# Kernel tuning notes

Hardware: AMD Instinct MI355X
Metric: run time of the kernel (lower is better)

Reference implementation:

```python
import jax, jax.numpy as jnp
import numpy as np
import math


def setup_inputs() -> dict:
    key = jax.random.key(0)
    kq, kk, kv = jax.random.split(key, 3)
    B, H, S, D = 8, 12, 4096, 64
    q = jax.random.normal(kq, (B, H, S, D), dtype=jnp.float32)
    k = jax.random.normal(kk, (B, H, S, D), dtype=jnp.float32)
    v = jax.random.normal(kv, (B, H, S, D), dtype=jnp.float32)
    return {"q": q, "k": k, "v": v}


def reference(q, k, v):
    B, H, S, D = q.shape
    topk = int(2 * math.sqrt(S))  # 128 for S=4096
    # importance = mean + std (torch.std is unbiased -> ddof=1)
    importance = q.mean(axis=-1) + jnp.std(q, axis=-1, ddof=1)  # [B,H,S]
    _, idx = jax.lax.top_k(importance, topk)  # [B,H,topk]
    idx_e = idx[..., None]  # [B,H,topk,1]
    q_s = jnp.take_along_axis(q, idx_e, axis=2)  # [B,H,topk,D]
    k_s = jnp.take_along_axis(k, idx_e, axis=2)
    v_s = jnp.take_along_axis(v, idx_e, axis=2)
    scores = jnp.einsum('bhtd,bhsd->bhts', q_s, k_s) / math.sqrt(D)
    attn = jax.nn.softmax(scores, axis=-1)
    out_s = jnp.einsum('bhts,bhsd->bhtd', attn, v_s)  # [B,H,topk,D]
    # scatter back into a full tensor (torch uses empty_like; we use zeros
    # for the unselected positions so the output is deterministic)
    bI = jnp.arange(B)[:, None, None]
    hI = jnp.arange(H)[None, :, None]
    out = jnp.zeros_like(v).at[bI, hI, idx].set(out_s)  # [B,H,S,D]
    Himg = int(math.sqrt(S))
    return out.reshape(B, -1, Himg, Himg)  # [B, H*D, Himg, Himg]
```

## Files before the change

### kernel.cpp

```cpp
#include <hip/hip_runtime.h>
#include <hip/hip_fp16.h>
#include <math.h>

#define BH_N 96
#define S_N 4096
#define D_N 64
#define TOPK 128

typedef unsigned long long ull;

__device__ __forceinline__ ull orderKey(double d) {
  ull u = (ull)__double_as_longlong(d);
  if (u & 0x8000000000000000ULL) u = ~u;
  else u |= 0x8000000000000000ULL;
  return u;
}

__global__ __launch_bounds__(256)
void imp_zero_kernel(const float* __restrict__ q, float* __restrict__ out,
                     ull* __restrict__ keys) {
  const int tid = threadIdx.x;
  const size_t off = (size_t)blockIdx.x * 1024 + (size_t)tid * 4;
  const float4 v = *reinterpret_cast<const float4*>(q + off);
  float4 z; z.x = z.y = z.z = z.w = 0.f;
  *reinterpret_cast<float4*>(out + off) = z;

  double s  = (double)v.x + (double)v.y + (double)v.z + (double)v.w;
  double ss = (double)v.x * v.x + (double)v.y * v.y +
              (double)v.z * v.z + (double)v.w * v.w;
#pragma unroll
  for (int m = 1; m < 16; m <<= 1) {
    s  += __shfl_xor(s, m, 64);
    ss += __shfl_xor(ss, m, 64);
  }
  if ((tid & 15) == 0) {
    double mean = s * (1.0 / 64.0);
    double var = (ss - s * s * (1.0 / 64.0)) * (1.0 / 63.0);
    if (var < 0.0) var = 0.0;
    keys[(size_t)blockIdx.x * 16 + (tid >> 4)] = orderKey(mean + sqrt(var));
  }
}

__global__ __launch_bounds__(256)
void sel_kernel(const ull* __restrict__ keys, int* __restrict__ idx_out) {
  __shared__ int hist[2][256];
  __shared__ int s_idx[TOPK];
  __shared__ int sD, sRem;
  __shared__ int s_cnt;

  const int tid = threadIdx.x;
  const int lane = tid & 63;
  const int wv = tid >> 6;
  const int bh = blockIdx.x;
  const ull* kb = keys + (size_t)bh * S_N;

  ull key[16];
#pragma unroll
  for (int i = 0; i < 16; ++i) key[i] = kb[i * 256 + tid];

  hist[0][tid] = 0;
  hist[1][tid] = 0;
  if (tid == 0) { s_cnt = 0; }
  __syncthreads();

  ull prefix = 0;
  int rem = TOPK;
  int p = 0;
#pragma unroll 1
  for (int b = 0; b < 8; ++b) {
    const int shift = 56 - 8 * b;
    if (b == 0) {
#pragma unroll
      for (int i = 0; i < 16; ++i)
        atomicAdd(&hist[p][(int)((key[i] >> 56) & 255ULL)], 1);
    } else {
#pragma unroll
      for (int i = 0; i < 16; ++i) {
        if (((key[i] ^ prefix) >> (shift + 8)) == 0)
          atomicAdd(&hist[p][(int)((key[i] >> shift) & 255ULL)], 1);
      }
    }
    __syncthreads();
    if (wv == 0) {
      int rloc = rem;
      for (int c = 0; c < 4; ++c) {
        int d = 255 - (c * 64 + lane);
        int cnt = hist[p][d];
        int pre = cnt;
#pragma unroll
        for (int m = 1; m < 64; m <<= 1) {
          int t = __shfl_up(pre, m, 64);
          if (lane >= m) pre += t;
        }
        int tot = __shfl(pre, 63, 64);
        if (rloc <= tot) {
          ull mask = __ballot(pre >= rloc);
          int l = __ffsll((long long)mask) - 1;
          int preL = __shfl(pre, l, 64);
          int cntL = __shfl(cnt, l, 64);
          if (lane == 0) { sD = 255 - (c * 64 + l); sRem = rloc - (preL - cntL); }
          break;
        }
        rloc -= tot;
      }
    } else {
      for (int j = tid - 64; j < 256; j += 192) hist[p ^ 1][j] = 0;
    }
    __syncthreads();
    prefix |= ((ull)sD) << shift;
    rem = sRem;
    p ^= 1;
  }
  const ull T = prefix;

#pragma unroll
  for (int i = 0; i < 16; ++i) {
    if (key[i] > T) {
      int slot = atomicAdd(&s_cnt, 1);
      s_idx[slot] = i * 256 + tid;
    }
  }
  __syncthreads();
  const int nsel = s_cnt;
  if (wv == 0) {
    int running = 0;
    for (int base = 0; base < S_N && running < rem; base += 64) {
      ull kk2 = kb[base + lane];
      ull mask = __ballot(kk2 == T);
      if (kk2 == T) {
        int below = __popcll(mask & ((1ULL << lane) - 1ULL));
        int pos = running + below;
        if (pos < rem) s_idx[nsel + pos] = base + lane;
      }
      running += __popcll(mask);
    }
  }
  __syncthreads();
  if (tid < TOPK) idx_out[bh * TOPK + tid] = s_idx[tid];
}

__global__ __launch_bounds__(256)
void attn_kernel(const float* __restrict__ q, const float* __restrict__ k,
                 const float* __restrict__ v, const int* __restrict__ idx_all,
                 float* __restrict__ out) {
  __shared__ __align__(16) float sQ[32 * 65];
  __shared__ __align__(16) float sB[64 * 65];
  __shared__ __align__(16) __half sP[32 * 132];
  __shared__ int s_idx[TOPK];

  const int tid = threadIdx.x;
  const int bh = blockIdx.x >> 2;
  const int sub = blockIdx.x & 3;
  if (tid < TOPK) s_idx[tid] = idx_all[bh * TOPK + tid];

  const size_t base = (size_t)bh * S_N * D_N;
  const int rgrp = tid >> 4;
  const int c4 = (tid & 15) * 4;
  const int rr = tid >> 4;
  const int cc = tid & 15;

  __syncthreads();

#pragma unroll
  for (int it = 0; it < 2; ++it) {
    int r = it * 16 + rgrp;
    int srow = s_idx[sub * 32 + r];
    float4 val = *reinterpret_cast<const float4*>(q + base + (size_t)srow * D_N + c4);
    sQ[r * 65 + c4 + 0] = val.x; sQ[r * 65 + c4 + 1] = val.y;
    sQ[r * 65 + c4 + 2] = val.z; sQ[r * 65 + c4 + 3] = val.w;
  }

  float acc[2][8];
#pragma unroll
  for (int j = 0; j < 2; ++j)
#pragma unroll
    for (int m = 0; m < 8; ++m) acc[j][m] = 0.f;

  for (int h = 0; h < 2; ++h) {
    __syncthreads();
#pragma unroll
    for (int it = 0; it < 4; ++it) {
      int r = it * 16 + rgrp;
      int srow = s_idx[h * 64 + r];
      float4 val = *reinterpret_cast<const float4*>(k + base + (size_t)srow * D_N + c4);
      sB[r * 65 + c4 + 0] = val.x; sB[r * 65 + c4 + 1] = val.y;
      sB[r * 65 + c4 + 2] = val.z; sB[r * 65 + c4 + 3] = val.w;
    }
    __syncthreads();
    for (int kk = 0; kk < 64; kk += 2) {
#pragma unroll
      for (int u = 0; u < 2; ++u) {
        float qv0 = sQ[(2 * rr + 0) * 65 + kk + u];
        float qv1 = sQ[(2 * rr + 1) * 65 + kk + u];
        float kv[4];
#pragma unroll
        for (int m = 0; m < 4; ++m) kv[m] = sB[(cc * 4 + m) * 65 + kk + u];
#pragma unroll
        for (int m = 0; m < 4; ++m) {
          acc[0][h * 4 + m] += qv0 * kv[m];
          acc[1][h * 4 + m] += qv1 * kv[m];
        }
      }
    }
  }

  float rmax[2], rsum[2];
#pragma unroll
  for (int j = 0; j < 2; ++j) {
    float mx = acc[j][0];
#pragma unroll
    for (int m = 1; m < 8; ++m) mx = fmaxf(mx, acc[j][m]);
    rmax[j] = mx;
  }
#pragma unroll
  for (int mm = 1; mm < 16; mm <<= 1)
#pragma unroll
    for (int j = 0; j < 2; ++j) rmax[j] = fmaxf(rmax[j], __shfl_xor(rmax[j], mm, 64));
#pragma unroll
  for (int j = 0; j < 2; ++j) {
    float sum = 0.f;
#pragma unroll
    for (int m = 0; m < 8; ++m) {
      float pe = __expf(0.125f * (acc[j][m] - rmax[j]));
      acc[j][m] = pe;
      sum += pe;
    }
    rsum[j] = sum;
  }
#pragma unroll
  for (int mm = 1; mm < 16; mm <<= 1)
#pragma unroll
    for (int j = 0; j < 2; ++j) rsum[j] += __shfl_xor(rsum[j], mm, 64);
#pragma unroll
  for (int j = 0; j < 2; ++j) {
    float rinv = 1.f / rsum[j];
#pragma unroll
    for (int h2 = 0; h2 < 2; ++h2)
#pragma unroll
      for (int m = 0; m < 4; ++m) {
        int col = h2 * 64 + cc * 4 + m;
        sP[(2 * rr + j) * 132 + col] = __float2half_rn(acc[j][h2 * 4 + m] * rinv);
      }
  }

  float acc2[2][4];
#pragma unroll
  for (int j = 0; j < 2; ++j)
#pragma unroll
    for (int m = 0; m < 4; ++m) acc2[j][m] = 0.f;

  for (int h = 0; h < 2; ++h) {
    __syncthreads();
#pragma unroll
    for (int it = 0; it < 4; ++it) {
      int r = it * 16 + rgrp;
      int srow = s_idx[h * 64 + r];
      float4 val = *reinterpret_cast<const float4*>(v + base + (size_t)srow * D_N + c4);
      sB[r * 65 + c4 + 0] = val.x; sB[r * 65 + c4 + 1] = val.y;
      sB[r * 65 + c4 + 2] = val.z; sB[r * 65 + c4 + 3] = val.w;
    }
    __syncthreads();
    for (int s2 = 0; s2 < 64; ++s2) {
      int scol = h * 64 + s2;
      float pj0 = __half2float(sP[(2 * rr + 0) * 132 + scol]);
      float pj1 = __half2float(sP[(2 * rr + 1) * 132 + scol]);
      float vm[4];
#pragma unroll
      for (int m = 0; m < 4; ++m) vm[m] = sB[s2 * 65 + cc * 4 + m];
#pragma unroll
      for (int m = 0; m < 4; ++m) {
        acc2[0][m] += pj0 * vm[m];
        acc2[1][m] += pj1 * vm[m];
      }
    }
  }

#pragma unroll
  for (int j = 0; j < 2; ++j) {
    int srow = s_idx[sub * 32 + 2 * rr + j];
    float4 val;
    val.x = acc2[j][0]; val.y = acc2[j][1]; val.z = acc2[j][2]; val.w = acc2[j][3];
    *reinterpret_cast<float4*>(out + base + (size_t)srow * D_N + cc * 4) = val;
  }
}

extern "C" void kernel_launch(void* const* d_in, const int* in_sizes, int n_in,
                              void* d_out, int out_size, void* d_ws, size_t ws_size,
                              hipStream_t stream) {
  const float* q = (const float*)d_in[0];
  const float* k = (const float*)d_in[1];
  const float* v = (const float*)d_in[2];
  float* out = (float*)d_out;
  ull* keys = (ull*)d_ws;
  int* idx = (int*)((char*)d_ws + (size_t)BH_N * S_N * 8);

  imp_zero_kernel<<<24576, 256, 0, stream>>>(q, out, keys);
  sel_kernel<<<BH_N, 256, 0, stream>>>(keys, idx);
  attn_kernel<<<BH_N * 4, 256, 0, stream>>>(q, k, v, idx, out);
}
```

Baseline: 311.3 us.

## Fuse top-k selection into attention kernel with deterministic ballot compaction

Merges the selection and attention kernels into one launch. Each of the four attention blocks per head recomputes the radix top-k selection redundantly instead of reading indices from a separate kernel. The atomic-based compaction and the serial tie scan over global memory are replaced by ballot-based prefix counting, which gives deterministic ordering. Shared-memory layouts are also changed to a stride-68 padding with transposed K so QK and PV can use float4 LDS reads. The cost is extra shared memory and a 4x duplication of selection work.

```diff
diff --git a/kernel.cpp b/kernel.cpp
--- a/kernel.cpp
+++ b/kernel.cpp
@@ -42,16 +42,22 @@
 }
 
 __global__ __launch_bounds__(256)
-void sel_kernel(const ull* __restrict__ keys, int* __restrict__ idx_out) {
+void fused_attn_kernel(const float* __restrict__ q, const float* __restrict__ k,
+                       const float* __restrict__ v, const ull* __restrict__ keys,
+                       float* __restrict__ out) {
   __shared__ int hist[2][256];
   __shared__ int s_idx[TOPK];
+  __shared__ int cntG[4][16], cntE[4][16];
   __shared__ int sD, sRem;
-  __shared__ int s_cnt;
+  __shared__ __align__(16) float sQ[32 * 68];
+  __shared__ __align__(16) float sKT[64 * 68];
+  __shared__ __align__(16) __half sP[32 * 132];
 
   const int tid = threadIdx.x;
   const int lane = tid & 63;
   const int wv = tid >> 6;
-  const int bh = blockIdx.x;
+  const int bh = blockIdx.x >> 2;
+  const int sub = blockIdx.x & 3;
   const ull* kb = keys + (size_t)bh * S_N;
 
   ull key[16];
@@ -60,7 +66,6 @@
 
   hist[0][tid] = 0;
   hist[1][tid] = 0;
-  if (tid == 0) { s_cnt = 0; }
   __syncthreads();
 
   ull prefix = 0;
@@ -112,46 +117,41 @@
     p ^= 1;
   }
   const ull T = prefix;
+  const int nselG = TOPK - rem;
 
 #pragma unroll
   for (int i = 0; i < 16; ++i) {
-    if (key[i] > T) {
-      int slot = atomicAdd(&s_cnt, 1);
-      s_idx[slot] = i * 256 + tid;
+    ull bg = __ballot(key[i] > T);
+    ull be = __ballot(key[i] == T);
+    if (lane == 0) {
+      cntG[wv][i] = __popcll(bg);
+      cntE[wv][i] = __popcll(be);
     }
   }
   __syncthreads();
-  const int nsel = s_cnt;
-  if (wv == 0) {
-    int running = 0;
-    for (int base = 0; base < S_N && running < rem; base += 64) {
-      ull kk2 = kb[base + lane];
-      ull mask = __ballot(kk2 == T);
-      if (kk2 == T) {
-        int below = __popcll(mask & ((1ULL << lane) - 1ULL));
-        int pos = running + below;
-        if (pos < rem) s_idx[nsel + pos] = base + lane;
-      }
-      running += __popcll(mask);
+  {
+    const ull below = (1ULL << lane) - 1ULL;
+    int baseG = 0, baseE = 0;
+#pragma unroll
+    for (int i = 0; i < 16; ++i) {
+      ull bg = __ballot(key[i] > T);
+      ull be = __ballot(key[i] == T);
+      int offG = baseG, offE = baseE;
+#pragma unroll
+      for (int w = 0; w < 4; ++w) {
+        int cg = cntG[w][i], ce = cntE[w][i];
+        if (w < wv) { offG += cg; offE += ce; }
+        baseG += cg; baseE += ce;
+      }
+      if (key[i] > T) {
+        s_idx[offG + __popcll(bg & below)] = i * 256 + tid;
+      } else if (key[i] == T) {
+        int tr = offE + __popcll(be & below);
+        if (tr < rem) s_idx[nselG + tr] = i * 256 + tid;
+      }
     }
   }
   __syncthreads();
-  if (tid < TOPK) idx_out[bh * TOPK + tid] = s_idx[tid];
-}
-
-__global__ __launch_bounds__(256)
-void attn_kernel(const float* __restrict__ q, const float* __restrict__ k,
-                 const float* __restrict__ v, const int* __restrict__ idx_all,
-                 float* __restrict__ out) {
-  __shared__ __align__(16) float sQ[32 * 65];
-  __shared__ __align__(16) float sB[64 * 65];
-  __shared__ __align__(16) __half sP[32 * 132];
-  __shared__ int s_idx[TOPK];
-
-  const int tid = threadIdx.x;
-  const int bh = blockIdx.x >> 2;
-  const int sub = blockIdx.x & 3;
-  if (tid < TOPK) s_idx[tid] = idx_all[bh * TOPK + tid];
 
   const size_t base = (size_t)bh * S_N * D_N;
   const int rgrp = tid >> 4;
@@ -159,15 +159,12 @@
   const int rr = tid >> 4;
   const int cc = tid & 15;
 
-  __syncthreads();
-
 #pragma unroll
   for (int it = 0; it < 2; ++it) {
     int r = it * 16 + rgrp;
     int srow = s_idx[sub * 32 + r];
     float4 val = *reinterpret_cast<const float4*>(q + base + (size_t)srow * D_N + c4);
-    sQ[r * 65 + c4 + 0] = val.x; sQ[r * 65 + c4 + 1] = val.y;
-    sQ[r * 65 + c4 + 2] = val.z; sQ[r * 65 + c4 + 3] = val.w;
+    *reinterpret_cast<float4*>(&sQ[r * 68 + c4]) = val;
   }
 
   float acc[2][8];
@@ -183,24 +180,20 @@
       int r = it * 16 + rgrp;
       int srow = s_idx[h * 64 + r];
       float4 val = *reinterpret_cast<const float4*>(k + base + (size_t)srow * D_N + c4);
-      sB[r * 65 + c4 + 0] = val.x; sB[r * 65 + c4 + 1] = val.y;
-      sB[r * 65 + c4 + 2] = val.z; sB[r * 65 + c4 + 3] = val.w;
-    }
-    __syncthreads();
-    for (int kk = 0; kk < 64; kk += 2) {
-#pragma unroll
-      for (int u = 0; u < 2; ++u) {
-        float qv0 = sQ[(2 * rr + 0) * 65 + kk + u];
-        float qv1 = sQ[(2 * rr + 1) * 65 + kk + u];
-        float kv[4];
-#pragma unroll
-        for (int m = 0; m < 4; ++m) kv[m] = sB[(cc * 4 + m) * 65 + kk + u];
-#pragma unroll
-        for (int m = 0; m < 4; ++m) {
-          acc[0][h * 4 + m] += qv0 * kv[m];
-          acc[1][h * 4 + m] += qv1 * kv[m];
-        }
-      }
+      sKT[(c4 + 0) * 68 + r] = val.x;
+      sKT[(c4 + 1) * 68 + r] = val.y;
+      sKT[(c4 + 2) * 68 + r] = val.z;
+      sKT[(c4 + 3) * 68 + r] = val.w;
+    }
+    __syncthreads();
+    for (int kk = 0; kk < 64; ++kk) {
+      float q0 = sQ[(2 * rr + 0) * 68 + kk];
+      float q1 = sQ[(2 * rr + 1) * 68 + kk];
+      float4 kx = *reinterpret_cast<const float4*>(&sKT[kk * 68 + 4 * cc]);
+      acc[0][h * 4 + 0] += q0 * kx.x; acc[0][h * 4 + 1] += q0 * kx.y;
+      acc[0][h * 4 + 2] += q0 * kx.z; acc[0][h * 4 + 3] += q0 * kx.w;
+      acc[1][h * 4 + 0] += q1 * kx.x; acc[1][h * 4 + 1] += q1 * kx.y;
+      acc[1][h * 4 + 2] += q1 * kx.z; acc[1][h * 4 + 3] += q1 * kx.w;
     }
   }
 
@@ -243,6 +236,7 @@
       }
   }
 
+  float* sV = sKT;
   float acc2[2][4];
 #pragma unroll
   for (int j = 0; j < 2; ++j)
@@ -256,22 +250,18 @@
       int r = it * 16 + rgrp;
       int srow = s_idx[h * 64 + r];
       float4 val = *reinterpret_cast<const float4*>(v + base + (size_t)srow * D_N + c4);
-      sB[r * 65 + c4 + 0] = val.x; sB[r * 65 + c4 + 1] = val.y;
-      sB[r * 65 + c4 + 2] = val.z; sB[r * 65 + c4 + 3] = val.w;
+      *reinterpret_cast<float4*>(&sV[r * 68 + c4]) = val;
     }
     __syncthreads();
     for (int s2 = 0; s2 < 64; ++s2) {
       int scol = h * 64 + s2;
-      float pj0 = __half2float(sP[(2 * rr + 0) * 132 + scol]);
-      float pj1 = __half2float(sP[(2 * rr + 1) * 132 + scol]);
-      float vm[4];
-#pragma unroll
-      for (int m = 0; m < 4; ++m) vm[m] = sB[s2 * 65 + cc * 4 + m];
-#pragma unroll
-      for (int m = 0; m < 4; ++m) {
-        acc2[0][m] += pj0 * vm[m];
-        acc2[1][m] += pj1 * vm[m];
-      }
+      float p0 = __half2float(sP[(2 * rr + 0) * 132 + scol]);
+      float p1 = __half2float(sP[(2 * rr + 1) * 132 + scol]);
+      float4 vv = *reinterpret_cast<const float4*>(&sV[s2 * 68 + 4 * cc]);
+      acc2[0][0] += p0 * vv.x; acc2[0][1] += p0 * vv.y;
+      acc2[0][2] += p0 * vv.z; acc2[0][3] += p0 * vv.w;
+      acc2[1][0] += p1 * vv.x; acc2[1][1] += p1 * vv.y;
+      acc2[1][2] += p1 * vv.z; acc2[1][3] += p1 * vv.w;
     }
   }
 
@@ -280,7 +270,7 @@
     int srow = s_idx[sub * 32 + 2 * rr + j];
     float4 val;
     val.x = acc2[j][0]; val.y = acc2[j][1]; val.z = acc2[j][2]; val.w = acc2[j][3];
-    *reinterpret_cast<float4*>(out + base + (size_t)srow * D_N + cc * 4) = val;
+    *reinterpret_cast<float4*>(out + base + (size_t)srow * D_N + 4 * cc) = val;
   }
 }
 
@@ -292,9 +282,7 @@
   const float* v = (const float*)d_in[2];
   float* out = (float*)d_out;
   ull* keys = (ull*)d_ws;
-  int* idx = (int*)((char*)d_ws + (size_t)BH_N * S_N * 8);
 
   imp_zero_kernel<<<24576, 256, 0, stream>>>(q, out, keys);
-  sel_kernel<<<BH_N, 256, 0, stream>>>(keys, idx);
-  attn_kernel<<<BH_N * 4, 256, 0, stream>>>(q, k, v, idx, out);
-}
+  fused_attn_kernel<<<BH_N * 4, 256, 0, stream>>>(q, k, v, keys, out);
+}
```

New measurement: 313.4 us. No clear change (+0.7%).
